# Kernel tuning notes

Measured on AMD Instinct MI355X. Metric: run time of the kernel, lower is better.

Reference implementation:

```python
import jax, jax.numpy as jnp
import numpy as np

N_U, N_D = 64, 64
N_E = N_U + N_D
N_A = 32
N_SV, N_PV = 512, 64
# n1 = [4*N_A, N_SV, N_SV, N_SV]; n2 = [4, N_PV, N_PV, N_PV]


def setup_inputs() -> dict:
    key = jax.random.key(0)
    ks = jax.random.split(key, 32)
    n1 = [4 * N_A, N_SV, N_SV, N_SV]
    n2 = [4, N_PV, N_PV, N_PV]
    d = {}
    d['r'] = jax.random.normal(ks[0], (N_E, 3), jnp.float32)
    d['a'] = jax.random.normal(ks[1], (N_A, 3), jnp.float32)
    i = 2
    for l in range(3):
        fin = 3 * n1[l] + 2 * n2[l]
        d[f'V{l}_w'] = jax.random.normal(ks[i], (fin, n1[l + 1]), jnp.float32) / np.float32(np.sqrt(fin)); i += 1
        d[f'V{l}_b'] = jax.random.normal(ks[i], (n1[l + 1],), jnp.float32); i += 1
        d[f'W{l}_w'] = jax.random.normal(ks[i], (n2[l], n2[l + 1]), jnp.float32) / np.float32(np.sqrt(n2[l])); i += 1
        d[f'W{l}_b'] = jax.random.normal(ks[i], (n2[l + 1],), jnp.float32); i += 1
    fin = 3 * N_SV + 2 * N_PV
    d['after_w'] = jax.random.normal(ks[i], (fin, N_SV), jnp.float32) / np.float32(np.sqrt(fin)); i += 1
    d['after_b'] = jax.random.normal(ks[i], (N_SV,), jnp.float32); i += 1
    d['vhu_w'] = jax.random.normal(ks[i], (N_SV, N_SV // 2), jnp.float32) / np.float32(np.sqrt(N_SV)); i += 1
    d['vhu_b'] = jax.random.normal(ks[i], (N_SV // 2,), jnp.float32); i += 1
    d['vhd_w'] = jax.random.normal(ks[i], (N_SV, N_SV // 2), jnp.float32) / np.float32(np.sqrt(N_SV)); i += 1
    d['vhd_b'] = jax.random.normal(ks[i], (N_SV // 2,), jnp.float32); i += 1
    d['wu_w'] = jax.random.normal(ks[i], (N_SV // 2, N_U), jnp.float32) / np.float32(np.sqrt(N_SV // 2)); i += 1
    d['wu_b'] = jax.random.normal(ks[i], (N_U,), jnp.float32); i += 1
    d['wd_w'] = jax.random.normal(ks[i], (N_SV // 2, N_D), jnp.float32) / np.float32(np.sqrt(N_SV // 2)); i += 1
    d['wd_b'] = jax.random.normal(ks[i], (N_D,), jnp.float32); i += 1
    return d


def _fb_block(s_v, p_v):
    # s_v: (N_E, f_s), p_v: (N_E, N_E, f_p)
    s_u_mean = jnp.tile(s_v[:N_U].mean(0)[None, :], (N_E, 1))
    s_d_mean = jnp.tile(s_v[N_U:].mean(0)[None, :], (N_E, 1))
    p_u_mean = p_v[:N_U].mean(0)  # (N_E, f_p)
    p_d_mean = p_v[N_U:].mean(0)
    return jnp.concatenate([s_u_mean, s_d_mean, p_u_mean, p_d_mean, s_v], axis=-1)


def _forward(r, a, Vw, Vb, Ww, Wb, after_w, after_b, vhu_w, vhu_b, vhd_w, vhd_b, wu_w, wu_b, wd_w, wd_b):
    eye = jnp.eye(N_E, dtype=r.dtype)[:, :, None]
    ra = r[:, None, :] - a[None, :, :]                       # (N_E, N_A, 3)
    ra_len = jnp.linalg.norm(ra, axis=-1, keepdims=True)     # (N_E, N_A, 1)
    rr = r[None, :, :] - r[:, None, :]                       # (N_E, N_E, 3)
    rr_len = jnp.linalg.norm(rr + eye, axis=-1, keepdims=True) * (1.0 - eye)
    s_v = jnp.concatenate([ra, ra_len], axis=-1).reshape(N_E, -1)  # (N_E, 4*N_A)
    p_v = jnp.concatenate([rr, rr_len], axis=-1)                   # (N_E, N_E, 4)
    for vw, vb, ww, wb in zip(Vw, Vb, Ww, Wb):
        s_in = _fb_block(s_v, p_v)
        # NOTE: torch residual `s_v if s_v.shape[-1]==n_sv` never fires here:
        # fb_block output width is 3*n1+2*n2 != n_sv, so it adds zeros.
        s_v = jnp.tanh(s_in @ vw + vb)
        p_new = jnp.tanh(p_v @ ww + wb)
        p_v = p_new + (p_v if p_v.shape[-1] == N_PV else 0.0)
    s_in = _fb_block(s_v, p_v)
    s_v = jnp.tanh(s_in @ after_w + after_b)  # (N_E, N_SV); residual again never fires
    s_u = s_v[:N_U] @ vhu_w + vhu_b
    s_d = s_v[N_U:] @ vhd_w + vhd_b
    s_wu = s_u @ wu_w + wu_b   # (N_U, N_U)
    s_wd = s_d @ wd_w + wd_b   # (N_D, N_D)
    exp_u = jnp.linalg.norm(ra[:N_U], axis=-1, keepdims=True)  # (N_U, N_A, 1)
    exp_d = jnp.linalg.norm(ra[N_U:], axis=-1, keepdims=True)
    orb_u = (s_wu * jnp.exp(-exp_u).sum(axis=1))[None]  # (1, N_U, N_U)
    orb_d = (s_wd * jnp.exp(-exp_d).sum(axis=1))[None]
    # logabssumdet for two (1,n,n) matrices with n>1: no 1x1 dets.
    sgn_u, ld_u = jnp.linalg.slogdet(orb_u)
    sgn_d, ld_d = jnp.linalg.slogdet(orb_d)
    sign = sgn_u * sgn_d
    logdet = ld_u + ld_d        # (1,)
    maxlogdet = logdet.max()
    psi = (sign * jnp.exp(logdet - maxlogdet)).sum()
    return jnp.log(jnp.abs(psi)) + maxlogdet  # scalar log|psi|


def reference(r, a, V0_w, V0_b, V1_w, V1_b, V2_w, V2_b, W0_w, W0_b, W1_w, W1_b, W2_w, W2_b,
              after_w, after_b, vhu_w, vhu_b, vhd_w, vhd_b, wu_w, wu_b, wd_w, wd_b):
    Vw, Vb = [V0_w, V1_w, V2_w], [V0_b, V1_b, V2_b]
    Ww, Wb = [W0_w, W1_w, W2_w], [W0_b, W1_b, W2_b]
    return _forward(r, a, Vw, Vb, Ww, Wb, after_w, after_b,
                    vhu_w, vhu_b, vhd_w, vhd_b, wu_w, wu_b, wd_w, wd_b)
```

## Files before the change

### kernel.cpp

```cpp
#include <hip/hip_runtime.h>
#include <math.h>

#define NSV 512

__device__ void pchain_role(int b, const float* __restrict__ r,
                            const float* __restrict__ apos,
                            const float* __restrict__ W0w, const float* __restrict__ W0b,
                            const float* __restrict__ W1w, const float* __restrict__ W1b,
                            const float* __restrict__ W2w, const float* __restrict__ W2b,
                            float* __restrict__ expv,
                            float* __restrict__ pme1, float* __restrict__ pme2,
                            float* __restrict__ pme3, float* sh)
{
    float* rL    = sh;
    float* W0l   = sh + 384;
    float* aposL = sh + 640;
    float* shex  = sh + 736;
    float* p0c   = sh + 768;
    float* PA    = sh + 1024;
    float* Wbuf  = sh + 5376;
    const int j  = b >> 1, sp = b & 1;
    const int t  = threadIdx.x;
    const int i  = t >> 3;
    const int o0 = (t & 7) * 8;

    if (t < 384) rL[t] = r[t];
    else if (t < 480) aposL[t - 384] = apos[t - 384];
    for (int idx = t; idx < 4096; idx += 512) Wbuf[idx] = W1w[idx];
    if (t < 256) W0l[t] = W0w[t];
    __syncthreads();

    const float rjx = rL[j*3+0], rjy = rL[j*3+1], rjz = rL[j*3+2];
    if (t < 64) {
        const int ii = sp*64 + t;
        float dx = rjx - rL[ii*3+0], dy = rjy - rL[ii*3+1], dz = rjz - rL[ii*3+2];
        float len = (ii == j) ? 0.f : sqrtf(dx*dx + dy*dy + dz*dz);
        p0c[t*4+0]=dx; p0c[t*4+1]=dy; p0c[t*4+2]=dz; p0c[t*4+3]=len;
    } else if (sp == 0 && t < 96) {
        const int k = t - 64;
        float dx = rjx - aposL[k*3+0], dy = rjy - aposL[k*3+1], dz = rjz - aposL[k*3+2];
        shex[k] = expf(-sqrtf(dx*dx + dy*dy + dz*dz));
    }
    __syncthreads();

    {
        const float x0=p0c[i*4+0], x1=p0c[i*4+1], x2=p0c[i*4+2], x3=p0c[i*4+3];
        #pragma unroll
        for (int k = 0; k < 8; ++k) {
            const int o = o0 + k;
            float a = W0b[o];
            a = fmaf(x0, W0l[o],     a);
            a = fmaf(x1, W0l[64+o],  a);
            a = fmaf(x2, W0l[128+o], a);
            a = fmaf(x3, W0l[192+o], a);
            PA[i*68+o] = tanhf(a);
        }
    }
    if (sp == 0 && t == 4) {
        float s = 0.f;
        #pragma unroll 8
        for (int k = 0; k < 32; ++k) s += shex[k];
        expv[j] = s;
    }
    __syncthreads();

    if (t < 64) {
        float s = 0.f;
        #pragma unroll 8
        for (int k = 0; k < 64; ++k) s += PA[k*68 + t];
        pme1[j*128 + sp*64 + t] = s * 0.015625f;
    }
    float acc[8], res[8];
    const float* pa = PA + i*68;
    {
        #pragma unroll
        for (int k = 0; k < 8; ++k) acc[k] = W1b[o0+k];
        #pragma unroll 4
        for (int c = 0; c < 64; ++c) {
            const float av = pa[c];
            const float* wr = Wbuf + c*64 + o0;
            float4 wa = *reinterpret_cast<const float4*>(wr);
            float4 wb = *reinterpret_cast<const float4*>(wr+4);
            acc[0]=fmaf(av,wa.x,acc[0]); acc[1]=fmaf(av,wa.y,acc[1]);
            acc[2]=fmaf(av,wa.z,acc[2]); acc[3]=fmaf(av,wa.w,acc[3]);
            acc[4]=fmaf(av,wb.x,acc[4]); acc[5]=fmaf(av,wb.y,acc[5]);
            acc[6]=fmaf(av,wb.z,acc[6]); acc[7]=fmaf(av,wb.w,acc[7]);
        }
        #pragma unroll
        for (int k = 0; k < 8; ++k) res[k] = pa[o0+k];
    }
    __syncthreads();
    #pragma unroll
    for (int k = 0; k < 8; ++k) PA[i*68+o0+k] = tanhf(acc[k]) + res[k];
    __syncthreads();

    if (t < 64) {
        float s = 0.f;
        #pragma unroll 8
        for (int k = 0; k < 64; ++k) s += PA[k*68 + t];
        pme2[j*128 + sp*64 + t] = s * 0.015625f;
    }
    for (int idx = t; idx < 4096; idx += 512) Wbuf[idx] = W2w[idx];
    __syncthreads();

    {
        #pragma unroll
        for (int k = 0; k < 8; ++k) acc[k] = W2b[o0+k];
        #pragma unroll 4
        for (int c = 0; c < 64; ++c) {
            const float av = pa[c];
            const float* wr = Wbuf + c*64 + o0;
            float4 wa = *reinterpret_cast<const float4*>(wr);
            float4 wb = *reinterpret_cast<const float4*>(wr+4);
            acc[0]=fmaf(av,wa.x,acc[0]); acc[1]=fmaf(av,wa.y,acc[1]);
            acc[2]=fmaf(av,wa.z,acc[2]); acc[3]=fmaf(av,wa.w,acc[3]);
            acc[4]=fmaf(av,wb.x,acc[4]); acc[5]=fmaf(av,wb.y,acc[5]);
            acc[6]=fmaf(av,wb.z,acc[6]); acc[7]=fmaf(av,wb.w,acc[7]);
        }
        #pragma unroll
        for (int k = 0; k < 8; ++k) res[k] = pa[o0+k];
    }
    __syncthreads();
    #pragma unroll
    for (int k = 0; k < 8; ++k) PA[i*68+o0+k] = tanhf(acc[k]) + res[k];
    __syncthreads();

    if (t < 64) {
        float s = 0.f;
        #pragma unroll 8
        for (int k = 0; k < 64; ++k) s += PA[k*68 + t];
        pme3[j*128 + sp*64 + t] = s * 0.015625f;
    }
}

__device__ void a0_role(int ab, const float* __restrict__ r,
                        const float* __restrict__ apos,
                        const float* __restrict__ V0w, const float* __restrict__ V0b,
                        float* __restrict__ svA, float* __restrict__ psA, float* sh)
{
    constexpr int KP = 136, KP2 = 68;
    float* As    = sh;
    float* smL   = sh + 544;
    float* red   = sh + 800;
    float* t1L   = sh + 1312;
    float* rL    = sh + 1376;
    float* aposL = sh + 1760;
    const int t  = threadIdx.x;
    const int et = ab >> 3, e0 = et * 4;
    const int o0 = (ab & 7) * 64;
    const int ol = t & 63, o = o0 + ol;
    const int wv = t >> 6;

    if (t < 384) rL[t] = r[t];
    else if (t < 480) aposL[t - 384] = apos[t - 384];
    __syncthreads();

    if (t < 128) {
        const int e_l = t >> 5, k = t & 31;
        const int e = e0 + e_l;
        float dx = rL[e*3+0]-aposL[k*3+0], dy = rL[e*3+1]-aposL[k*3+1],
              dz = rL[e*3+2]-aposL[k*3+2];
        float len = sqrtf(dx*dx + dy*dy + dz*dz);
        float* dst = As + e_l*KP + 8 + k*4;
        dst[0]=dx; dst[1]=dy; dst[2]=dz; dst[3]=len;
    } else if (t < 160) {
        const int q = t - 128;
        const int e_l = q >> 3, outp = q & 7;
        const int spin = outp >> 2, c = outp & 3;
        const int e = e0 + e_l;
        const float ex = rL[e*3+0], ey = rL[e*3+1], ez = rL[e*3+2];
        float s = 0.f;
        for (int i2 = 0; i2 < 64; ++i2) {
            const int ii = spin*64 + i2;
            float dx = ex - rL[ii*3+0], dy = ey - rL[ii*3+1], dz = ez - rL[ii*3+2];
            float v = (c==0)?dx:(c==1)?dy:(c==2)?dz:
                      ((ii==e)?0.f:sqrtf(dx*dx+dy*dy+dz*dz));
            s += v;
        }
        As[e_l*KP + outp] = s * 0.015625f;
    }
    {
        const int outp = t >> 1, half = t & 1;
        const int spin = outp >> 7, cc = outp & 127, a_i = cc >> 2, d = cc & 3;
        const float ax = aposL[a_i*3+0], ay = aposL[a_i*3+1], az = aposL[a_i*3+2];
        float s = 0.f;
        #pragma unroll 8
        for (int q = 0; q < 32; ++q) {
            const int e = spin*64 + half*32 + q;
            float dx = rL[e*3+0]-ax, dy = rL[e*3+1]-ay, dz = rL[e*3+2]-az;
            float len = sqrtf(dx*dx + dy*dy + dz*dz);
            s += (d==0)?dx:(d==1)?dy:(d==2)?dz:len;
        }
        red[t] = s;
    }
    __syncthreads();
    if (t < 256) smL[t] = (red[2*t] + red[2*t+1]) * 0.015625f;
    __syncthreads();

    {
        float a1 = 0.f;
        const float* Wp = V0w + (size_t)(wv*32)*NSV + o;
        const float* mp = smL + wv*32;
        #pragma unroll 8
        for (int k = 0; k < 32; ++k) a1 = fmaf(mp[k], Wp[(size_t)k*NSV], a1);
        red[wv*64 + ol] = a1;
    }
    __syncthreads();
    if (t < 64) {
        float s = V0b[o0 + t];
        #pragma unroll
        for (int g = 0; g < 8; ++g) s += red[g*64 + t];
        t1L[t] = s;
    }
    __syncthreads();

    const int e_l = wv & 3, kh = wv >> 2;
    {
        float a2 = (kh == 0) ? t1L[ol] : 0.f;
        const float* Ap = As + e_l*KP + kh*KP2;
        const float* Wp = V0w + (size_t)(256 + kh*KP2)*NSV + o;
        #pragma unroll 16
        for (int k = 0; k < KP2; ++k)
            a2 = fmaf(Ap[k], Wp[(size_t)k*NSV], a2);
        red[wv*64 + ol] = a2;
    }
    __syncthreads();
    float v = 0.f;
    if (t < 256) {
        v = tanhf(red[(t>>6)*64 + (t&63)] + red[((t>>6)+4)*64 + (t&63)]);
        svA[(size_t)(e0 + (t>>6))*NSV + o0 + (t&63)] = v;
    }
    __syncthreads();
    if (t < 256) red[t] = v;
    __syncthreads();
    if (t < 64) {
        float s = red[t] + red[64+t] + red[128+t] + red[192+t];
        psA[(size_t)et*NSV + o0 + t] = s;
    }
}

__device__ void headc_role(int g, const float* __restrict__ vh,
                           const float* __restrict__ wu,
                           float* __restrict__ Cdst, float* sh)
{
    float* wuL = sh;
    float* vhL = sh + 4096;
    const int t = threadIdx.x;
    const int o2 = t & 63, wq = t >> 6;
    const int f0 = g * 16;
    float a0 = 0.f, a1 = 0.f;
    for (int hc = 0; hc < 4; ++hc) {
        __syncthreads();
        for (int idx = t; idx < 4096; idx += 512)
            wuL[idx] = wu[(size_t)(hc*64 + (idx>>6))*64 + (idx&63)];
        for (int idx = t; idx < 1024; idx += 512)
            vhL[idx] = vh[(size_t)(f0 + (idx>>6))*256 + hc*64 + (idx&63)];
        __syncthreads();
        #pragma unroll 8
        for (int h = 0; h < 64; ++h) {
            const float wuv = wuL[h*64 + o2];
            a0 = fmaf(vhL[wq*64 + h],     wuv, a0);
            a1 = fmaf(vhL[(wq+8)*64 + h], wuv, a1);
        }
    }
    Cdst[(size_t)(f0 + wq)*64 + o2]     = a0;
    Cdst[(size_t)(f0 + wq + 8)*64 + o2] = a1;
}

__device__ void cb_role(const float* __restrict__ vhb, const float* __restrict__ wu,
                        const float* __restrict__ wub, float* __restrict__ cbdst,
                        float* sh)
{
    const int t = threadIdx.x;
    const int o2 = t & 63, wq = t >> 6;
    float acc = 0.f;
    #pragma unroll
    for (int k = 0; k < 32; ++k) {
        const int h = wq*32 + k;
        acc = fmaf(vhb[h], wu[(size_t)h*64 + o2], acc);
    }
    sh[t] = acc;
    __syncthreads();
    if (t < 64) {
        float s = wub[t];
        #pragma unroll
        for (int g = 0; g < 8; ++g) s += sh[g*64 + t];
        cbdst[t] = s;
    }
}

__global__ __launch_bounds__(512)
void front_kernel(const float* __restrict__ r, const float* __restrict__ apos,
                  const float* __restrict__ V0w, const float* __restrict__ V0b,
                  const float* __restrict__ W0w, const float* __restrict__ W0b,
                  const float* __restrict__ W1w, const float* __restrict__ W1b,
                  const float* __restrict__ W2w, const float* __restrict__ W2b,
                  const float* __restrict__ vhuw, const float* __restrict__ vhub,
                  const float* __restrict__ vhdw, const float* __restrict__ vhdb,
                  const float* __restrict__ wuw,  const float* __restrict__ wub,
                  const float* __restrict__ wdw,  const float* __restrict__ wdb,
                  float* __restrict__ svA, float* __restrict__ expv,
                  float* __restrict__ pme1, float* __restrict__ pme2,
                  float* __restrict__ pme3, float* __restrict__ psA,
                  float* __restrict__ Cmat, float* __restrict__ cb)
{
    __shared__ __align__(16) float sh[9472];
    const int b = blockIdx.x;
    if (b < 256) {
        pchain_role(b, r, apos, W0w, W0b, W1w, W1b, W2w, W2b,
                    expv, pme1, pme2, pme3, sh);
    } else if (b < 512) {
        a0_role(b - 256, r, apos, V0w, V0b, svA, psA, sh);
    } else if (b < 576) {
        const int g = b - 512;
        const int spin = g >> 5;
        headc_role(g & 31, spin ? vhdw : vhuw, spin ? wdw : wuw,
                   Cmat + (size_t)spin*32768, sh);
    } else {
        const int spin = b - 576;
        cb_role(spin ? vhdb : vhub, spin ? wdw : wuw, spin ? wdb : wub,
                cb + spin*64, sh);
    }
}

template<int FS, int FP>
__global__ __launch_bounds__(512)
void a2_kernel(const float* __restrict__ svIn, const float* __restrict__ pmeIn,
               const float* __restrict__ psumIn,
               const float* __restrict__ Vw, const float* __restrict__ Vb,
               float* __restrict__ svOut, float* __restrict__ psumOut,
               float* __restrict__ orbInit, const float* __restrict__ cb)
{
    constexpr int KP  = 2*FP + FS;
    constexpr int KP2 = KP/2;
    __shared__ __align__(16) float As[4*KP];
    __shared__ __align__(16) float smL[2*FS];
    __shared__ __align__(16) float red[512];
    __shared__ float t1L[64];
    const int t  = threadIdx.x;
    if (blockIdx.x >= 256) {
        for (int idx = t; idx < 8192; idx += 512)
            orbInit[idx] = cb[(((idx >> 6) >> 6) << 6) + (idx & 63)];
        return;
    }
    const int et = blockIdx.x >> 3;
    const int e0 = et * 4;
    const int o0 = (blockIdx.x & 7) * 64;
    const int ol = t & 63;
    const int o  = o0 + ol;
    const int wv = t >> 6;

    for (int idx = t; idx < 4*2*FP; idx += 512)
        As[(idx/(2*FP))*KP + idx%(2*FP)] =
            pmeIn[(size_t)(e0 + idx/(2*FP))*(2*FP) + idx%(2*FP)];
    for (int idx = t; idx < FS; idx += 512) {
        const int row = idx / (FS/4), c4 = idx % (FS/4);
        *reinterpret_cast<float4*>(&As[row*KP + 2*FP + c4*4]) =
            *reinterpret_cast<const float4*>(&svIn[(size_t)(e0+row)*FS + c4*4]);
    }
    for (int idx = t; idx < 2*FS; idx += 512) {
        const int col = (idx < FS) ? idx : idx - FS;
        const int r0  = (idx < FS) ? 0 : 16;
        const float* base = psumIn + (size_t)r0*NSV + col;
        float s = 0.f;
        #pragma unroll
        for (int k = 0; k < 16; ++k) s += base[(size_t)k*NSV];
        smL[idx] = s * 0.015625f;
    }
    __syncthreads();

    {
        constexpr int TI = (2*FS)/8;
        const float* Wp = Vw + (size_t)(wv*TI)*NSV + o;
        const float* mp = smL + wv*TI;
        float p0=0.f, p1=0.f, p2=0.f, p3=0.f;
        #pragma unroll 4
        for (int k = 0; k < TI; k += 4) {
            p0 = fmaf(mp[k],   Wp[(size_t)(k  )*NSV], p0);
            p1 = fmaf(mp[k+1], Wp[(size_t)(k+1)*NSV], p1);
            p2 = fmaf(mp[k+2], Wp[(size_t)(k+2)*NSV], p2);
            p3 = fmaf(mp[k+3], Wp[(size_t)(k+3)*NSV], p3);
        }
        red[wv*64 + ol] = (p0 + p1) + (p2 + p3);
    }
    __syncthreads();
    if (t < 64) {
        float s = Vb[o0 + t];
        #pragma unroll
        for (int g = 0; g < 8; ++g) s += red[g*64 + t];
        t1L[t] = s;
    }
    __syncthreads();

    const int e_l = wv & 3, kh = wv >> 2;
    {
        const float* Ap = As + e_l*KP + kh*KP2;
        const float* Wp = Vw + (size_t)(2*FS + kh*KP2)*NSV + o;
        float s0 = (kh == 0) ? t1L[ol] : 0.f;
        float s1=0.f, s2=0.f, s3=0.f;
        #pragma unroll 8
        for (int k = 0; k < KP2; k += 4) {
            s0 = fmaf(Ap[k],   Wp[(size_t)(k  )*NSV], s0);
            s1 = fmaf(Ap[k+1], Wp[(size_t)(k+1)*NSV], s1);
            s2 = fmaf(Ap[k+2], Wp[(size_t)(k+2)*NSV], s2);
            s3 = fmaf(Ap[k+3], Wp[(size_t)(k+3)*NSV], s3);
        }
        red[wv*64 + ol] = (s0 + s1) + (s2 + s3);
    }
    __syncthreads();
    float v = 0.f;
    if (t < 256) {
        v = tanhf(red[(t>>6)*64 + (t&63)] + red[((t>>6)+4)*64 + (t&63)]);
        svOut[(size_t)(e0 + (t>>6))*NSV + o0 + (t&63)] = v;
    }
    if (psumOut) {
        __syncthreads();
        if (t < 256) red[t] = v;
        __syncthreads();
        if (t < 64) {
            float s = red[t] + red[64+t] + red[128+t] + red[192+t];
            psumOut[(size_t)et*NSV + o0 + t] = s;
        }
    }
}

__global__ __launch_bounds__(512)
void a3h_kernel(const float* __restrict__ svIn, const float* __restrict__ pmeIn,
                const float* __restrict__ psumIn,
                const float* __restrict__ Vw, const float* __restrict__ Vb,
                const float* __restrict__ Cmat, float* __restrict__ orb)
{
    constexpr int FS = 512, FP = 64;
    constexpr int KP  = 2*FP + FS;
    constexpr int KP2 = KP/2;
    __shared__ __align__(16) float As[4*KP];
    __shared__ __align__(16) float smL[2*FS];
    __shared__ __align__(16) float red[512];
    __shared__ float t1L[64];
    const int t  = threadIdx.x;
    const int et = blockIdx.x >> 3;
    const int e0 = et * 4;
    const int o0 = (blockIdx.x & 7) * 64;
    const int ol = t & 63;
    const int o  = o0 + ol;
    const int wv = t >> 6;

    for (int idx = t; idx < 4*2*FP; idx += 512)
        As[(idx/(2*FP))*KP + idx%(2*FP)] =
            pmeIn[(size_t)(e0 + idx/(2*FP))*(2*FP) + idx%(2*FP)];
    for (int idx = t; idx < FS; idx += 512) {
        const int row = idx / (FS/4), c4 = idx % (FS/4);
        *reinterpret_cast<float4*>(&As[row*KP + 2*FP + c4*4]) =
            *reinterpret_cast<const float4*>(&svIn[(size_t)(e0+row)*FS + c4*4]);
    }
    for (int idx = t; idx < 2*FS; idx += 512) {
        const int col = (idx < FS) ? idx : idx - FS;
        const int r0  = (idx < FS) ? 0 : 16;
        const float* base = psumIn + (size_t)r0*NSV + col;
        float s = 0.f;
        #pragma unroll
        for (int k = 0; k < 16; ++k) s += base[(size_t)k*NSV];
        smL[idx] = s * 0.015625f;
    }
    __syncthreads();

    {
        constexpr int TI = (2*FS)/8;
        const float* Wp = Vw + (size_t)(wv*TI)*NSV + o;
        const float* mp = smL + wv*TI;
        float p0=0.f, p1=0.f, p2=0.f, p3=0.f;
        #pragma unroll 4
        for (int k = 0; k < TI; k += 4) {
            p0 = fmaf(mp[k],   Wp[(size_t)(k  )*NSV], p0);
            p1 = fmaf(mp[k+1], Wp[(size_t)(k+1)*NSV], p1);
            p2 = fmaf(mp[k+2], Wp[(size_t)(k+2)*NSV], p2);
            p3 = fmaf(mp[k+3], Wp[(size_t)(k+3)*NSV], p3);
        }
        red[wv*64 + ol] = (p0 + p1) + (p2 + p3);
    }
    __syncthreads();
    if (t < 64) {
        float s = Vb[o0 + t];
        #pragma unroll
        for (int g = 0; g < 8; ++g) s += red[g*64 + t];
        t1L[t] = s;
    }
    __syncthreads();

    const int e_l = wv & 3, kh = wv >> 2;
    {
        const float* Ap = As + e_l*KP + kh*KP2;
        const float* Wp = Vw + (size_t)(2*FS + kh*KP2)*NSV + o;
        float s0 = (kh == 0) ? t1L[ol] : 0.f;
        float s1=0.f, s2=0.f, s3=0.f;
        #pragma unroll 8
        for (int k = 0; k < KP2; k += 4) {
            s0 = fmaf(Ap[k],   Wp[(size_t)(k  )*NSV], s0);
            s1 = fmaf(Ap[k+1], Wp[(size_t)(k+1)*NSV], s1);
            s2 = fmaf(Ap[k+2], Wp[(size_t)(k+2)*NSV], s2);
            s3 = fmaf(Ap[k+3], Wp[(size_t)(k+3)*NSV], s3);
        }
        red[wv*64 + ol] = (s0 + s1) + (s2 + s3);
    }
    __syncthreads();
    float v = 0.f;
    if (t < 256)
        v = tanhf(red[(t>>6)*64 + (t&63)] + red[((t>>6)+4)*64 + (t&63)]);
    __syncthreads();
    if (t < 256) smL[t] = v;
    __syncthreads();
    if (t < 256) {
        const int el2 = t >> 6, o2 = t & 63;
        const int spin = et >> 4;
        const float* Cp = Cmat + (size_t)spin*32768 + (size_t)o0*64 + o2;
        const float* sp = smL + el2*64;
        float acc = 0.f;
        #pragma unroll 8
        for (int f = 0; f < 64; ++f)
            acc = fmaf(sp[f], Cp[(size_t)f*64], acc);
        atomicAdd(&orb[(size_t)(e0 + el2)*64 + o2], acc);
    }
}

__device__ __forceinline__ int imax2(int a, int b) { return a > b ? a : b; }
__device__ __forceinline__ float readlane_f(float x, int lane) {
    return __int_as_float(__builtin_amdgcn_readlane(__float_as_int(x), lane));
}

__global__ __launch_bounds__(128)
void det_kernel(const float* __restrict__ orb, const float* __restrict__ expv,
                float* __restrict__ out)
{
    __shared__ float parts[2];
    const int t = threadIdx.x;
    const int w = t >> 6;
    const int lane = t & 63;
    const float* M = orb + (size_t)w*4096 + (size_t)lane*64;
    const float ex = expv[w*64 + lane];
    float rr[64];
    #pragma unroll
    for (int j = 0; j < 64; j += 4) {
        float4 v = *reinterpret_cast<const float4*>(M + j);
        rr[j]=v.x*ex; rr[j+1]=v.y*ex; rr[j+2]=v.z*ex; rr[j+3]=v.w*ex;
    }
    float pv_mine = 1.f;
    bool active = true;
    #pragma unroll
    for (int k = 0; k < 64; ++k) {
        int bits = (int)(__float_as_uint(rr[k]) & 0x7FFFFFC0u);
        int v = active ? (bits | lane) : lane;
        int tmp;
        tmp = __builtin_amdgcn_update_dpp(0, v, 0xB1,  0xF, 0xF, true); v = imax2(v, tmp);
        tmp = __builtin_amdgcn_update_dpp(0, v, 0x4E,  0xF, 0xF, true); v = imax2(v, tmp);
        tmp = __builtin_amdgcn_update_dpp(0, v, 0x141, 0xF, 0xF, true); v = imax2(v, tmp);
        tmp = __builtin_amdgcn_update_dpp(0, v, 0x140, 0xF, 0xF, true); v = imax2(v, tmp);
        tmp = __builtin_amdgcn_update_dpp(0, v, 0x142, 0xF, 0xF, true); v = imax2(v, tmp);
        tmp = __builtin_amdgcn_update_dpp(0, v, 0x143, 0xF, 0xF, true); v = imax2(v, tmp);
        const int idx = __builtin_amdgcn_readlane(v, 63) & 63;
        const float piv = readlane_f(rr[k], idx);
        pv_mine = (lane == k) ? piv : pv_mine;
        const float linv = __builtin_amdgcn_rcpf(piv);
        const float l = (active && lane != idx) ? rr[k]*linv : 0.f;
        if (lane == idx) active = false;
        #pragma unroll
        for (int j = k+1; j < 64; ++j)
            rr[j] = fmaf(-l, readlane_f(rr[j], idx), rr[j]);
    }
    float lg = logf(fabsf(pv_mine));
    #pragma unroll
    for (int off = 32; off; off >>= 1) lg += __shfl_down(lg, off);
    if (lane == 0) parts[w] = lg;
    __syncthreads();
    if (t == 0) out[0] = parts[0] + parts[1];
}

extern "C" void kernel_launch(void* const* d_in, const int* in_sizes, int n_in,
                              void* d_out, int out_size, void* d_ws, size_t ws_size,
                              hipStream_t stream)
{
    const float* r    = (const float*)d_in[0];
    const float* apos = (const float*)d_in[1];
    const float* V0w  = (const float*)d_in[2];
    const float* V0b  = (const float*)d_in[3];
    const float* W0w  = (const float*)d_in[4];
    const float* W0b  = (const float*)d_in[5];
    const float* V1w  = (const float*)d_in[6];
    const float* V1b  = (const float*)d_in[7];
    const float* W1w  = (const float*)d_in[8];
    const float* W1b  = (const float*)d_in[9];
    const float* V2w  = (const float*)d_in[10];
    const float* V2b  = (const float*)d_in[11];
    const float* W2w  = (const float*)d_in[12];
    const float* W2b  = (const float*)d_in[13];
    const float* afw  = (const float*)d_in[14];
    const float* afb  = (const float*)d_in[15];
    const float* vhuw = (const float*)d_in[16];
    const float* vhub = (const float*)d_in[17];
    const float* vhdw = (const float*)d_in[18];
    const float* vhdb = (const float*)d_in[19];
    const float* wuw  = (const float*)d_in[20];
    const float* wub  = (const float*)d_in[21];
    const float* wdw  = (const float*)d_in[22];
    const float* wdb  = (const float*)d_in[23];

    float* ws   = (float*)d_ws;
    float* svA  = ws;
    float* svB  = svA  + 65536;
    float* expv = svB  + 65536;
    float* pme1 = expv + 128;
    float* pme2 = pme1 + 16384;
    float* pme3 = pme2 + 16384;
    float* psA  = pme3 + 16384;
    float* psB  = psA  + 16384;
    float* orb  = psB  + 16384;
    float* Cmat = orb  + 8192;
    float* cb   = Cmat + 65536;

    front_kernel<<<578, 512, 0, stream>>>(r, apos, V0w, V0b, W0w, W0b,
                                          W1w, W1b, W2w, W2b,
                                          vhuw, vhub, vhdw, vhdb,
                                          wuw, wub, wdw, wdb,
                                          svA, expv, pme1, pme2, pme3, psA,
                                          Cmat, cb);
    a2_kernel<512, 64><<<257, 512, 0, stream>>>(svA, pme1, psA, V1w, V1b,
                                                svB, psB, orb, cb);
    a2_kernel<512, 64><<<256, 512, 0, stream>>>(svB, pme2, psB, V2w, V2b,
                                                svA, psA, nullptr, nullptr);
    a3h_kernel<<<256, 512, 0, stream>>>(svA, pme3, psA, afw, afb, Cmat, orb);
    det_kernel<<<1, 128, 0, stream>>>(orb, expv, (float*)d_out);
}
```

Baseline: 89.33 us.

## Halve electrons per block in layer kernels to double grid parallelism

The a2 and a3h kernels now handle 2 electrons per block instead of 4 and launch twice as many blocks (512). The K dimension is split four ways across waves instead of two. The partial-sum buffers grow to 64 rows, so the next layer's mean reduction reads 32 rows per half instead of 16. The aim is to fill more CUs on the device, at the cost of reading each weight column twice as often and doing more reduction work.

After: 96.56 us. 1.08x slower.

```diff
diff --git a/kernel.cpp b/kernel.cpp
--- a/kernel.cpp
+++ b/kernel.cpp
@@ -136,7 +136,7 @@
 __device__ void a0_role(int ab, const float* __restrict__ r,
                         const float* __restrict__ apos,
                         const float* __restrict__ V0w, const float* __restrict__ V0b,
-                        float* __restrict__ svA, float* __restrict__ psA, float* sh)
+                        float* __restrict__ svA, float* __restrict__ ps0, float* sh)
 {
     constexpr int KP = 136, KP2 = 68;
     float* As    = sh;
@@ -235,7 +235,7 @@
     __syncthreads();
     if (t < 64) {
         float s = red[t] + red[64+t] + red[128+t] + red[192+t];
-        psA[(size_t)et*NSV + o0 + t] = s;
+        ps0[(size_t)et*NSV + o0 + t] = s;
     }
 }
 
@@ -301,7 +301,7 @@
                   const float* __restrict__ wdw,  const float* __restrict__ wdb,
                   float* __restrict__ svA, float* __restrict__ expv,
                   float* __restrict__ pme1, float* __restrict__ pme2,
-                  float* __restrict__ pme3, float* __restrict__ psA,
+                  float* __restrict__ pme3, float* __restrict__ ps0,
                   float* __restrict__ Cmat, float* __restrict__ cb)
 {
     __shared__ __align__(16) float sh[9472];
@@ -310,7 +310,7 @@
         pchain_role(b, r, apos, W0w, W0b, W1w, W1b, W2w, W2b,
                     expv, pme1, pme2, pme3, sh);
     } else if (b < 512) {
-        a0_role(b - 256, r, apos, V0w, V0b, svA, psA, sh);
+        a0_role(b - 256, r, apos, V0w, V0b, svA, ps0, sh);
     } else if (b < 576) {
         const int g = b - 512;
         const int spin = g >> 5;
@@ -323,7 +323,7 @@
     }
 }
 
-template<int FS, int FP>
+template<int FS, int FP, int RIN>
 __global__ __launch_bounds__(512)
 void a2_kernel(const float* __restrict__ svIn, const float* __restrict__ pmeIn,
                const float* __restrict__ psumIn,
@@ -332,39 +332,39 @@
                float* __restrict__ orbInit, const float* __restrict__ cb)
 {
     constexpr int KP  = 2*FP + FS;
-    constexpr int KP2 = KP/2;
-    __shared__ __align__(16) float As[4*KP];
+    constexpr int KP4 = KP/4;
+    __shared__ __align__(16) float As[2*KP];
     __shared__ __align__(16) float smL[2*FS];
     __shared__ __align__(16) float red[512];
     __shared__ float t1L[64];
     const int t  = threadIdx.x;
-    if (blockIdx.x >= 256) {
+    if (blockIdx.x >= 512) {
         for (int idx = t; idx < 8192; idx += 512)
             orbInit[idx] = cb[(((idx >> 6) >> 6) << 6) + (idx & 63)];
         return;
     }
     const int et = blockIdx.x >> 3;
-    const int e0 = et * 4;
+    const int e0 = et * 2;
     const int o0 = (blockIdx.x & 7) * 64;
     const int ol = t & 63;
     const int o  = o0 + ol;
     const int wv = t >> 6;
 
-    for (int idx = t; idx < 4*2*FP; idx += 512)
+    for (int idx = t; idx < 2*2*FP; idx += 512)
         As[(idx/(2*FP))*KP + idx%(2*FP)] =
             pmeIn[(size_t)(e0 + idx/(2*FP))*(2*FP) + idx%(2*FP)];
-    for (int idx = t; idx < FS; idx += 512) {
+    for (int idx = t; idx < FS/2; idx += 512) {
         const int row = idx / (FS/4), c4 = idx % (FS/4);
         *reinterpret_cast<float4*>(&As[row*KP + 2*FP + c4*4]) =
             *reinterpret_cast<const float4*>(&svIn[(size_t)(e0+row)*FS + c4*4]);
     }
     for (int idx = t; idx < 2*FS; idx += 512) {
         const int col = (idx < FS) ? idx : idx - FS;
-        const int r0  = (idx < FS) ? 0 : 16;
+        const int r0  = (idx < FS) ? 0 : RIN/2;
         const float* base = psumIn + (size_t)r0*NSV + col;
         float s = 0.f;
         #pragma unroll
-        for (int k = 0; k < 16; ++k) s += base[(size_t)k*NSV];
+        for (int k = 0; k < RIN/2; ++k) s += base[(size_t)k*NSV];
         smL[idx] = s * 0.015625f;
     }
     __syncthreads();
@@ -392,14 +392,14 @@
     }
     __syncthreads();
 
-    const int e_l = wv & 3, kh = wv >> 2;
-    {
-        const float* Ap = As + e_l*KP + kh*KP2;
-        const float* Wp = Vw + (size_t)(2*FS + kh*KP2)*NSV + o;
+    const int e_l = wv & 1, kh = wv >> 1;
+    {
+        const float* Ap = As + e_l*KP + kh*KP4;
+        const float* Wp = Vw + (size_t)(2*FS + kh*KP4)*NSV + o;
         float s0 = (kh == 0) ? t1L[ol] : 0.f;
         float s1=0.f, s2=0.f, s3=0.f;
         #pragma unroll 8
-        for (int k = 0; k < KP2; k += 4) {
+        for (int k = 0; k < KP4; k += 4) {
             s0 = fmaf(Ap[k],   Wp[(size_t)(k  )*NSV], s0);
             s1 = fmaf(Ap[k+1], Wp[(size_t)(k+1)*NSV], s1);
             s2 = fmaf(Ap[k+2], Wp[(size_t)(k+2)*NSV], s2);
@@ -409,18 +409,17 @@
     }
     __syncthreads();
     float v = 0.f;
-    if (t < 256) {
-        v = tanhf(red[(t>>6)*64 + (t&63)] + red[((t>>6)+4)*64 + (t&63)]);
-        svOut[(size_t)(e0 + (t>>6))*NSV + o0 + (t&63)] = v;
-    }
-    if (psumOut) {
-        __syncthreads();
-        if (t < 256) red[t] = v;
-        __syncthreads();
-        if (t < 64) {
-            float s = red[t] + red[64+t] + red[128+t] + red[192+t];
-            psumOut[(size_t)et*NSV + o0 + t] = s;
-        }
+    if (t < 128) {
+        const int el2 = t >> 6, oo = t & 63;
+        v = tanhf((red[el2*64 + oo]       + red[(2+el2)*64 + oo]) +
+                  (red[(4+el2)*64 + oo]   + red[(6+el2)*64 + oo]));
+        svOut[(size_t)(e0 + el2)*NSV + o0 + oo] = v;
+    }
+    __syncthreads();
+    if (t < 128) smL[t] = v;
+    __syncthreads();
+    if (t < 64) {
+        psumOut[(size_t)et*NSV + o0 + t] = smL[t] + smL[64 + t];
     }
 }
 
@@ -432,34 +431,34 @@
 {
     constexpr int FS = 512, FP = 64;
     constexpr int KP  = 2*FP + FS;
-    constexpr int KP2 = KP/2;
-    __shared__ __align__(16) float As[4*KP];
+    constexpr int KP4 = KP/4;
+    __shared__ __align__(16) float As[2*KP];
     __shared__ __align__(16) float smL[2*FS];
     __shared__ __align__(16) float red[512];
     __shared__ float t1L[64];
     const int t  = threadIdx.x;
     const int et = blockIdx.x >> 3;
-    const int e0 = et * 4;
+    const int e0 = et * 2;
     const int o0 = (blockIdx.x & 7) * 64;
     const int ol = t & 63;
     const int o  = o0 + ol;
     const int wv = t >> 6;
 
-    for (int idx = t; idx < 4*2*FP; idx += 512)
+    for (int idx = t; idx < 2*2*FP; idx += 512)
         As[(idx/(2*FP))*KP + idx%(2*FP)] =
             pmeIn[(size_t)(e0 + idx/(2*FP))*(2*FP) + idx%(2*FP)];
-    for (int idx = t; idx < FS; idx += 512) {
+    for (int idx = t; idx < FS/2; idx += 512) {
         const int row = idx / (FS/4), c4 = idx % (FS/4);
         *reinterpret_cast<float4*>(&As[row*KP + 2*FP + c4*4]) =
             *reinterpret_cast<const float4*>(&svIn[(size_t)(e0+row)*FS + c4*4]);
     }
     for (int idx = t; idx < 2*FS; idx += 512) {
         const int col = (idx < FS) ? idx : idx - FS;
-        const int r0  = (idx < FS) ? 0 : 16;
+        const int r0  = (idx < FS) ? 0 : 32;
         const float* base = psumIn + (size_t)r0*NSV + col;
         float s = 0.f;
         #pragma unroll
-        for (int k = 0; k < 16; ++k) s += base[(size_t)k*NSV];
+        for (int k = 0; k < 32; ++k) s += base[(size_t)k*NSV];
         smL[idx] = s * 0.015625f;
     }
     __syncthreads();
@@ -487,14 +486,14 @@
     }
     __syncthreads();
 
-    const int e_l = wv & 3, kh = wv >> 2;
-    {
-        const float* Ap = As + e_l*KP + kh*KP2;
-        const float* Wp = Vw + (size_t)(2*FS + kh*KP2)*NSV + o;
+    const int e_l = wv & 1, kh = wv >> 1;
+    {
+        const float* Ap = As + e_l*KP + kh*KP4;
+        const float* Wp = Vw + (size_t)(2*FS + kh*KP4)*NSV + o;
         float s0 = (kh == 0) ? t1L[ol] : 0.f;
         float s1=0.f, s2=0.f, s3=0.f;
         #pragma unroll 8
-        for (int k = 0; k < KP2; k += 4) {
+        for (int k = 0; k < KP4; k += 4) {
             s0 = fmaf(Ap[k],   Wp[(size_t)(k  )*NSV], s0);
             s1 = fmaf(Ap[k+1], Wp[(size_t)(k+1)*NSV], s1);
             s2 = fmaf(Ap[k+2], Wp[(size_t)(k+2)*NSV], s2);
@@ -504,14 +503,17 @@
     }
     __syncthreads();
     float v = 0.f;
-    if (t < 256)
-        v = tanhf(red[(t>>6)*64 + (t&63)] + red[((t>>6)+4)*64 + (t&63)]);
-    __syncthreads();
-    if (t < 256) smL[t] = v;
-    __syncthreads();
-    if (t < 256) {
+    if (t < 128) {
+        const int el2 = t >> 6, oo = t & 63;
+        v = tanhf((red[el2*64 + oo]     + red[(2+el2)*64 + oo]) +
+                  (red[(4+el2)*64 + oo] + red[(6+el2)*64 + oo]));
+    }
+    __syncthreads();
+    if (t < 128) smL[t] = v;
+    __syncthreads();
+    if (t < 128) {
         const int el2 = t >> 6, o2 = t & 63;
-        const int spin = et >> 4;
+        const int spin = et >> 5;
         const float* Cp = Cmat + (size_t)spin*32768 + (size_t)o0*64 + o2;
         const float* sp = smL + el2*64;
         float acc = 0.f;
@@ -610,9 +612,10 @@
     float* pme1 = expv + 128;
     float* pme2 = pme1 + 16384;
     float* pme3 = pme2 + 16384;
-    float* psA  = pme3 + 16384;
-    float* psB  = psA  + 16384;
-    float* orb  = psB  + 16384;
+    float* ps0  = pme3 + 16384;
+    float* psB  = ps0  + 16384;
+    float* psC  = psB  + 32768;
+    float* orb  = psC  + 32768;
     float* Cmat = orb  + 8192;
     float* cb   = Cmat + 65536;
 
@@ -620,12 +623,12 @@
                                           W1w, W1b, W2w, W2b,
                                           vhuw, vhub, vhdw, vhdb,
                                           wuw, wub, wdw, wdb,
-                                          svA, expv, pme1, pme2, pme3, psA,
+                                          svA, expv, pme1, pme2, pme3, ps0,
                                           Cmat, cb);
-    a2_kernel<512, 64><<<257, 512, 0, stream>>>(svA, pme1, psA, V1w, V1b,
-                                                svB, psB, orb, cb);
-    a2_kernel<512, 64><<<256, 512, 0, stream>>>(svB, pme2, psB, V2w, V2b,
-                                                svA, psA, nullptr, nullptr);
-    a3h_kernel<<<256, 512, 0, stream>>>(svA, pme3, psA, afw, afb, Cmat, orb);
+    a2_kernel<512, 64, 32><<<513, 512, 0, stream>>>(svA, pme1, ps0, V1w, V1b,
+                                                    svB, psB, orb, cb);
+    a2_kernel<512, 64, 64><<<512, 512, 0, stream>>>(svB, pme2, psB, V2w, V2b,
+                                                    svA, psC, nullptr, nullptr);
+    a3h_kernel<<<512, 512, 0, stream>>>(svA, pme3, psC, afw, afb, Cmat, orb);
     det_kernel<<<1, 128, 0, stream>>>(orb, expv, (float*)d_out);
 }
```
